# Optimization experiments

Hardware: AMD Instinct MI355X
Metric: run time of the kernel (lower is better)

The kernel has to match this reference:

```python
import jax, jax.numpy as jnp
import numpy as np

B, N, P, D = 32, 8, 6, 96
E, H, I, K, NL = 128, 8, 64, 32, 2
L = N * D  # transformer sequence length = 768
OUT = 128
EPS = 1e-5


def _layernorm(x, s, b):
    m = jnp.mean(x, axis=-1, keepdims=True)
    v = jnp.mean((x - m) ** 2, axis=-1, keepdims=True)
    return (x - m) / jnp.sqrt(v + EPS) * s + b


def _pos_encoding(length, d_model):
    pos = jnp.arange(length, dtype=jnp.float32)[:, None]
    div = jnp.exp(jnp.arange(0, d_model, 2, dtype=jnp.float32) * (-jnp.log(10000.0) / d_model))
    ang = pos * div  # [L, E/2]
    return jnp.stack([jnp.sin(ang), jnp.cos(ang)], axis=-1).reshape(length, d_model)


def setup_inputs() -> dict:
    key = jax.random.key(0)
    ks = jax.random.split(key, 20)
    s = 0.02
    return {
        "x": jax.random.normal(ks[0], (B, N, P, D), jnp.float32),
        "prototypes": jax.random.normal(ks[1], (D, K, P), jnp.float32),
        "emb_w": jax.random.normal(ks[2], (E, P), jnp.float32) * s,
        "emb_b": jnp.zeros((E,), jnp.float32),
        "proj_w": jax.random.normal(ks[3], (E, P), jnp.float32) * s,
        "proj_b": jnp.zeros((E,), jnp.float32),
        "in_proj_w": jax.random.normal(ks[4], (NL, 3 * E, E), jnp.float32) * s,
        "in_proj_b": jnp.zeros((NL, 3 * E), jnp.float32),
        "out_proj_w": jax.random.normal(ks[5], (NL, E, E), jnp.float32) * s,
        "out_proj_b": jnp.zeros((NL, E), jnp.float32),
        "ln1_s": jnp.ones((NL, E), jnp.float32),
        "ln1_b": jnp.zeros((NL, E), jnp.float32),
        "ffn_w1": jax.random.normal(ks[6], (NL, I, E), jnp.float32) * s,
        "ffn_b1": jnp.zeros((NL, I), jnp.float32),
        "ffn_w2": jax.random.normal(ks[7], (NL, E, I), jnp.float32) * s,
        "ffn_b2": jnp.zeros((NL, E), jnp.float32),
        "ln2_s": jnp.ones((NL, E), jnp.float32),
        "ln2_b": jnp.zeros((NL, E), jnp.float32),
        "out_w": jax.random.normal(ks[8], (OUT, L * E), jnp.float32) * s,
        "out_b": jnp.zeros((OUT,), jnp.float32),
    }


def reference(x, prototypes, emb_w, emb_b, proj_w, proj_b,
              in_proj_w, in_proj_b, out_proj_w, out_proj_b,
              ln1_s, ln1_b, ffn_w1, ffn_b1, ffn_w2, ffn_b2,
              ln2_s, ln2_b, out_w, out_b):
    # Faithful to torch .view: raw row-major reinterpretation [B,N,P,D] -> [B*N*D, P]
    x_flat = x.reshape(B * N * D, P)
    x_normed = x_flat / jnp.maximum(jnp.linalg.norm(x_flat, axis=1, keepdims=True), 1e-12)
    x_norm = x_normed.reshape(B, N, D, P)
    p_normed = prototypes / jnp.maximum(jnp.linalg.norm(prototypes, axis=2, keepdims=True), 1e-12)

    # Vectorized per-dim cosine-sim argmax + gather (replaces the Python loop over D)
    sim = jnp.einsum('bndp,dkp->bndk', x_norm, p_normed)  # [B,N,D,K]
    best_idx = jnp.argmax(sim, axis=3)                    # [B,N,D]
    d_idx = jnp.arange(D)[None, None, :]
    selected = p_normed[d_idx, best_idx]                  # [B,N,D,P]

    input_embed = (x_flat @ emb_w.T + emb_b).reshape(B, N, D, E)
    proto_embed = (selected.reshape(B * N * D, P) @ proj_w.T + proj_b).reshape(B, N, D, E)
    seq = (input_embed + proto_embed).reshape(B, L, E)
    seq = seq + _pos_encoding(L, E)[None]

    scale = 1.0 / jnp.sqrt(jnp.float32(E // H))
    for l in range(NL):
        qkv = seq @ in_proj_w[l].T + in_proj_b[l]          # [B,L,3E]
        q, k, v = jnp.split(qkv, 3, axis=-1)
        q = q.reshape(B, L, H, E // H)
        k = k.reshape(B, L, H, E // H)
        v = v.reshape(B, L, H, E // H)
        logits = jnp.einsum('blhd,bmhd->bhlm', q, k) * scale
        attn = jax.nn.softmax(logits, axis=-1)
        ctx = jnp.einsum('bhlm,bmhd->blhd', attn, v).reshape(B, L, E)
        attn_out = ctx @ out_proj_w[l].T + out_proj_b[l]
        seq = _layernorm(seq + attn_out, ln1_s[l], ln1_b[l])
        h = jax.nn.elu(seq @ ffn_w1[l].T + ffn_b1[l])
        ffn_out = h @ ffn_w2[l].T + ffn_b2[l]
        seq = _layernorm(seq + ffn_out, ln2_s[l], ln2_b[l])

    z = seq.reshape(B, L * E)
    return z @ out_w.T + out_b
```

## Files before the change

kernel.cpp:

```cpp
#include <hip/hip_runtime.h>
#include <hip/hip_bf16.h>
#include <math.h>

typedef unsigned short ushort_t;
typedef unsigned int uint_t;

#define BB 32
#define PP 6
#define DD 96
#define EE 128
#define HH 8
#define II 64
#define KK 32
#define LSEQ 768
#define ROWS (BB * LSEQ)
#define OUTN 128
#define KOUT (LSEQ * EE)

using bf16x8 = __attribute__((ext_vector_type(8))) short;
using bf16x4 = __attribute__((ext_vector_type(4))) short;
using f32x4  = __attribute__((ext_vector_type(4))) float;
using u32x4  = __attribute__((ext_vector_type(4))) uint_t;

__device__ __forceinline__ ushort_t f2b(float f) {
    __hip_bfloat16 h = __float2bfloat16(f);
    return *reinterpret_cast<ushort_t*>(&h);
}
__device__ __forceinline__ uint_t permpack(float hi, float lo) {
    return __builtin_amdgcn_perm(__builtin_bit_cast(uint_t, hi),
                                 __builtin_bit_cast(uint_t, lo), 0x07060302u);
}

#define NCAST 320
__global__ __launch_bounds__(512) void cast_embed_kernel(
    const float* __restrict__ s0, int n0, const float* __restrict__ s1, int n1,
    const float* __restrict__ s2, int n2, const float* __restrict__ s3, int n3,
    ushort_t* __restrict__ d0, ushort_t* __restrict__ d1,
    ushort_t* __restrict__ d2, ushort_t* __restrict__ d3,
    const float* __restrict__ x, const float* __restrict__ prot,
    const float* __restrict__ emb_w, const float* __restrict__ emb_b,
    const float* __restrict__ proj_w, const float* __restrict__ proj_b,
    float* __restrict__ seq, ushort_t* __restrict__ seq_bf)
{
    if (blockIdx.x < NCAST) {
        int i = blockIdx.x * 512 + threadIdx.x;
        if (i < n0) { d0[i] = f2b(s0[i]); return; }
        i -= n0;
        if (i < n1) { d1[i] = f2b(s1[i]); return; }
        i -= n1;
        if (i < n2) { d2[i] = f2b(s2[i]); return; }
        i -= n2;
        if (i < n3) { d3[i] = f2b(s3[i]); }
        return;
    }

    const int wave = threadIdx.x >> 6, lane = threadIdx.x & 63;
    const int r = (blockIdx.x - NCAST) * 8 + wave;
    const int d = r % DD;
    const int lpos = r % LSEQ;

    float xr[PP];
    float nx = 0.f;
    #pragma unroll
    for (int p = 0; p < PP; ++p) { xr[p] = x[r * PP + p]; nx += xr[p] * xr[p]; }
    const float xinv = 1.f / fmaxf(sqrtf(nx), 1e-12f);

    const int tk = lane & 31;
    const float* pr = prot + (d * KK + tk) * PP;
    float np2 = 0.f, dot = 0.f;
    #pragma unroll
    for (int p = 0; p < PP; ++p) {
        float pv = pr[p];
        np2 += pv * pv;
        dot += xr[p] * pv;
    }
    const float pinv = 1.f / fmaxf(sqrtf(np2), 1e-12f);
    float sim = dot * xinv * pinv;
    int k = tk;
    #pragma unroll
    for (int off = 16; off; off >>= 1) {
        float osim = __shfl_xor(sim, off);
        int   ok   = __shfl_xor(k, off);
        if (osim > sim || (osim == sim && ok < k)) { sim = osim; k = ok; }
    }
    const float* sr = prot + (d * KK + k) * PP;
    float sp[PP], sn2 = 0.f;
    #pragma unroll
    for (int p = 0; p < PP; ++p) { sp[p] = sr[p]; sn2 += sp[p] * sp[p]; }
    const float spinv = 1.f / fmaxf(sqrtf(sn2), 1e-12f);

    #pragma unroll
    for (int c = 0; c < 2; ++c) {
        const int t = lane + c * 64;
        float acc = emb_b[t] + proj_b[t];
        #pragma unroll
        for (int p = 0; p < PP; ++p) {
            acc = fmaf(xr[p], emb_w[t * PP + p], acc);
            acc = fmaf(sp[p] * spinv, proj_w[t * PP + p], acc);
        }
        const float twoj = (float)((t >> 1) * 2);
        const float div = __expf(twoj * (-9.210340371976184f / 128.0f));
        const float ang = (float)lpos * div;
        const float pe = (t & 1) ? __cosf(ang) : __sinf(ang);
        const float v = acc + pe;
        seq[(size_t)r * EE + t] = v;
        seq_bf[(size_t)r * EE + t] = f2b(v);
    }
}

__global__ __launch_bounds__(256) void gemm_qkv(
    const ushort_t* __restrict__ A, const ushort_t* __restrict__ W,
    const float* __restrict__ bias,
    ushort_t* __restrict__ q_bf, ushort_t* __restrict__ k2,
    ushort_t* __restrict__ v2)
{
    __shared__ ushort_t Ws[64 * 136];
    const int t = threadIdx.x;
    const int wave = t >> 6, lane = t & 63;
    const int quad = lane >> 4, l16 = lane & 15;
    const int m0 = blockIdx.y * 128, n0 = blockIdx.x * 64;

    for (int c = t; c < 64 * 16; c += 256) {
        int row = c >> 4, col = c & 15;
        *(bf16x8*)&Ws[row * 136 + col * 8] =
            *(const bf16x8*)&W[(size_t)(n0 + row) * 128 + col * 8];
    }
    __syncthreads();

    f32x4 acc[2][4];
    #pragma unroll
    for (int s = 0; s < 2; ++s)
        #pragma unroll
        for (int nt = 0; nt < 4; ++nt)
            acc[s][nt] = (f32x4){0.f, 0.f, 0.f, 0.f};

    const ushort_t* a0p = A + (size_t)(m0 + wave * 32 + l16) * 128 + quad * 8;
    const ushort_t* a1p = a0p + (size_t)16 * 128;
    const ushort_t* wp  = &Ws[l16 * 136 + quad * 8];

    #pragma unroll
    for (int k0 = 0; k0 < 128; k0 += 32) {
        bf16x8 a0 = *(const bf16x8*)(a0p + k0);
        bf16x8 a1 = *(const bf16x8*)(a1p + k0);
        #pragma unroll
        for (int nt = 0; nt < 4; ++nt) {
            bf16x8 wf = *(const bf16x8*)(wp + nt * 16 * 136 + k0);
            acc[0][nt] = __builtin_amdgcn_mfma_f32_16x16x32_bf16(wf, a0, acc[0][nt], 0, 0, 0);
            acc[1][nt] = __builtin_amdgcn_mfma_f32_16x16x32_bf16(wf, a1, acc[1][nt], 0, 0, 0);
        }
    }

    const int b = blockIdx.y / 6;
    #pragma unroll
    for (int s = 0; s < 2; ++s) {
        const int m = m0 + wave * 32 + s * 16 + l16;
        const int l = m - b * LSEQ;
        const int c32 = l >> 5, u = l & 31;
        #pragma unroll
        for (int nt = 0; nt < 4; ++nt) {
            const int nb = n0 + nt * 16 + quad * 4;
            float4 b4 = *(const float4*)&bias[nb];
            float v[4];
            #pragma unroll
            for (int r = 0; r < 4; ++r)
                v[r] = acc[s][nt][r] + ((const float*)&b4)[r];

            if (n0 < 128) {
                #pragma unroll
                for (int r = 0; r < 4; ++r) v[r] *= 0.36067376022224085f;
                uint2 w2;
                w2.x = permpack(v[1], v[0]);
                w2.y = permpack(v[3], v[2]);
                *(uint2*)&q_bf[(size_t)m * EE + nb] = w2;
            } else if (n0 < 256) {
                const int h = ((n0 - 128) >> 4) + nt;
                const int half = (u >> 2) & 1;
                const int mm = ((u >> 3) << 2) | (u & 3);
                uint2 w2;
                w2.x = permpack(v[1], v[0]);
                w2.y = permpack(v[3], v[2]);
                *(uint2*)&k2[((((((size_t)(b * HH + h)) * 24 + c32) * 2 + half) * 4 + quad) * 16 + mm) * 4] = w2;
            } else {
                const int h = ((n0 - 256) >> 4) + nt;
                const size_t vb = (((size_t)(b * HH + h)) * 24 + c32) * 512;
                #pragma unroll
                for (int r = 0; r < 4; ++r)
                    v2[vb + (quad * 4 + r) * 32 + u] = f2b(v[r]);
            }
        }
    }
}

__device__ __forceinline__ void attn_step32(
    bf16x4 kf0, bf16x4 kf1, bf16x8 vf, const bf16x4 (&qf)[2],
    f32x4 (&oacc)[2], f32x4 (&lacc)[2], bf16x8 ones8)
{
    const f32x4 zero4 = (f32x4){0.f, 0.f, 0.f, 0.f};
    #pragma unroll
    for (int s = 0; s < 2; ++s) {
        f32x4 sv0 = __builtin_amdgcn_mfma_f32_16x16x16bf16_1k(kf0, qf[s], zero4, 0, 0, 0);
        f32x4 sv1 = __builtin_amdgcn_mfma_f32_16x16x16bf16_1k(kf1, qf[s], zero4, 0, 0, 0);
        float e0 = __builtin_amdgcn_exp2f(sv0[0]);
        float e1 = __builtin_amdgcn_exp2f(sv0[1]);
        float e2 = __builtin_amdgcn_exp2f(sv0[2]);
        float e3 = __builtin_amdgcn_exp2f(sv0[3]);
        float e4 = __builtin_amdgcn_exp2f(sv1[0]);
        float e5 = __builtin_amdgcn_exp2f(sv1[1]);
        float e6 = __builtin_amdgcn_exp2f(sv1[2]);
        float e7 = __builtin_amdgcn_exp2f(sv1[3]);
        u32x4 pu;
        pu[0] = permpack(e1, e0);
        pu[1] = permpack(e3, e2);
        pu[2] = permpack(e5, e4);
        pu[3] = permpack(e7, e6);
        bf16x8 pf = __builtin_bit_cast(bf16x8, pu);
        oacc[s] = __builtin_amdgcn_mfma_f32_16x16x32_bf16(vf, pf, oacc[s], 0, 0, 0);
        lacc[s] = __builtin_amdgcn_mfma_f32_16x16x32_bf16(ones8, pf, lacc[s], 0, 0, 0);
    }
}

__global__ __launch_bounds__(256) void attention_mfma(
    const ushort_t* __restrict__ q_bf, const ushort_t* __restrict__ k2,
    const ushort_t* __restrict__ v2, ushort_t* __restrict__ ctx)
{
    const int bh = blockIdx.x;
    const int b = bh & 31, h = bh >> 5;
    const int qb = blockIdx.y;
    const int t = threadIdx.x;
    const int wave = t >> 6, lane = t & 63;
    const int quad = lane >> 4, l16 = lane & 15;
    const int hoff = h * 16;

    bf16x4 qf[2];
    #pragma unroll
    for (int s = 0; s < 2; ++s) {
        int row = b * LSEQ + qb * 128 + wave * 32 + s * 16 + l16;
        qf[s] = *(const bf16x4*)&q_bf[(size_t)row * EE + hoff + quad * 4];
    }

    const int bhn = b * HH + h;
    const ushort_t* kp = k2 + (size_t)bhn * 12288 + quad * 64 + l16 * 4;
    const ushort_t* vp = v2 + (size_t)bhn * 12288 + l16 * 32 + quad * 8;

    f32x4 oacc[2], lacc[2];
    oacc[0] = (f32x4){0.f, 0.f, 0.f, 0.f};
    oacc[1] = (f32x4){0.f, 0.f, 0.f, 0.f};
    lacc[0] = (f32x4){0.f, 0.f, 0.f, 0.f};
    lacc[1] = (f32x4){0.f, 0.f, 0.f, 0.f};
    bf16x8 ones8;
    #pragma unroll
    for (int j = 0; j < 8; ++j) ones8[j] = (short)0x3F80;

    bf16x4 k0a = *(const bf16x4*)(kp);
    bf16x4 k1a = *(const bf16x4*)(kp + 256);
    bf16x8 va  = *(const bf16x8*)(vp);
    bf16x4 k0b = *(const bf16x4*)(kp + 512);
    bf16x4 k1b = *(const bf16x4*)(kp + 768);
    bf16x8 vb  = *(const bf16x8*)(vp + 512);
    bf16x4 k0c = *(const bf16x4*)(kp + 1024);
    bf16x4 k1c = *(const bf16x4*)(kp + 1280);
    bf16x8 vc  = *(const bf16x8*)(vp + 1024);

    for (int c0 = 0; c0 < 24; c0 += 3) {
        attn_step32(k0a, k1a, va, qf, oacc, lacc, ones8);
        { int n = c0 + 3; if (n >= 24) n -= 24;
          k0a = *(const bf16x4*)(kp + n * 512);
          k1a = *(const bf16x4*)(kp + n * 512 + 256);
          va  = *(const bf16x8*)(vp + n * 512); }
        attn_step32(k0b, k1b, vb, qf, oacc, lacc, ones8);
        { int n = c0 + 4; if (n >= 24) n -= 24;
          k0b = *(const bf16x4*)(kp + n * 512);
          k1b = *(const bf16x4*)(kp + n * 512 + 256);
          vb  = *(const bf16x8*)(vp + n * 512); }
        attn_step32(k0c, k1c, vc, qf, oacc, lacc, ones8);
        { int n = c0 + 5; if (n >= 24) n -= 24;
          k0c = *(const bf16x4*)(kp + n * 512);
          k1c = *(const bf16x4*)(kp + n * 512 + 256);
          vc  = *(const bf16x8*)(vp + n * 512); }
    }

    #pragma unroll
    for (int s = 0; s < 2; ++s) {
        const float inv = 1.f / lacc[s][0];
        const int q = qb * 128 + wave * 32 + s * 16 + l16;
        uint2 w2;
        w2.x = permpack(oacc[s][1] * inv, oacc[s][0] * inv);
        w2.y = permpack(oacc[s][3] * inv, oacc[s][2] * inv);
        *(uint2*)&ctx[((size_t)(b * LSEQ + q)) * EE + hoff + quad * 4] = w2;
    }
}

#define W1OFF 0
#define W2OFF 8704
#define YOFF  17920
#define HOFF  26624
__global__ __launch_bounds__(256) void gemm_ln_ffn(
    const ushort_t* __restrict__ ctx_bf, const ushort_t* __restrict__ Wout,
    const float* __restrict__ bout,
    const float* __restrict__ g1, const float* __restrict__ be1,
    const ushort_t* __restrict__ W1, const float* __restrict__ b1,
    const ushort_t* __restrict__ W2, const float* __restrict__ b2,
    const float* __restrict__ g2, const float* __restrict__ be2,
    float* __restrict__ seq, ushort_t* __restrict__ seq_bf, int write_f32)
{
    __shared__ ushort_t S[31232];
    const int t = threadIdx.x;
    const int wave = t >> 6, lane = t & 63;
    const int quad = lane >> 4, l16 = lane & 15;
    const int m0 = blockIdx.x * 64;
    const int lrow = wave * 16 + l16;
    const int m = m0 + lrow;

    for (int c = t; c < 128 * 16; c += 256) {
        int row = c >> 4, col = c & 15;
        *(bf16x8*)&S[row * 136 + col * 8] =
            *(const bf16x8*)&Wout[(size_t)row * 128 + col * 8];
    }
    __syncthreads();

    f32x4 acc[8];
    #pragma unroll
    for (int nt = 0; nt < 8; ++nt) acc[nt] = (f32x4){0.f, 0.f, 0.f, 0.f};
    {
        const ushort_t* ap = ctx_bf + (size_t)m * EE + quad * 8;
        const ushort_t* wp = &S[l16 * 136 + quad * 8];
        #pragma unroll
        for (int k0 = 0; k0 < 128; k0 += 32) {
            bf16x8 a = *(const bf16x8*)(ap + k0);
            #pragma unroll
            for (int nt = 0; nt < 8; ++nt) {
                bf16x8 wf = *(const bf16x8*)(wp + nt * 16 * 136 + k0);
                acc[nt] = __builtin_amdgcn_mfma_f32_16x16x32_bf16(wf, a, acc[nt], 0, 0, 0);
            }
        }
    }
    __syncthreads();

    for (int c = t; c < 64 * 16; c += 256) {
        int row = c >> 4, col = c & 15;
        *(bf16x8*)&S[W1OFF + row * 136 + col * 8] =
            *(const bf16x8*)&W1[(size_t)row * 128 + col * 8];
    }
    for (int c = t; c < 128 * 8; c += 256) {
        int row = c >> 3, col = c & 7;
        *(bf16x8*)&S[W2OFF + row * 72 + col * 8] =
            *(const bf16x8*)&W2[(size_t)row * 64 + col * 8];
    }

    float y[8][4];
    float s = 0.f;
    #pragma unroll
    for (int nt = 0; nt < 8; ++nt) {
        const int nb = nt * 16 + quad * 4;
        float4 b4 = *(const float4*)&bout[nb];
        float4 r4 = *(const float4*)&seq[(size_t)m * EE + nb];
        #pragma unroll
        for (int r = 0; r < 4; ++r) {
            y[nt][r] = acc[nt][r] + ((const float*)&b4)[r] + ((const float*)&r4)[r];
            s += y[nt][r];
        }
    }
    s += __shfl_xor(s, 16);
    s += __shfl_xor(s, 32);
    float mean = s * (1.f / 128.f);
    float s2 = 0.f;
    #pragma unroll
    for (int nt = 0; nt < 8; ++nt)
        #pragma unroll
        for (int r = 0; r < 4; ++r) {
            float d = y[nt][r] - mean;
            s2 += d * d;
        }
    s2 += __shfl_xor(s2, 16);
    s2 += __shfl_xor(s2, 32);
    float rstd = 1.f / sqrtf(s2 * (1.f / 128.f) + 1e-5f);

    #pragma unroll
    for (int nt = 0; nt < 8; ++nt) {
        const int nb = nt * 16 + quad * 4;
        float4 g4 = *(const float4*)&g1[nb];
        float4 be4 = *(const float4*)&be1[nb];
        #pragma unroll
        for (int r = 0; r < 4; ++r)
            y[nt][r] = (y[nt][r] - mean) * rstd * ((const float*)&g4)[r] + ((const float*)&be4)[r];
        uint2 w2;
        w2.x = permpack(y[nt][1], y[nt][0]);
        w2.y = permpack(y[nt][3], y[nt][2]);
        *(uint2*)&S[YOFF + lrow * 136 + nb] = w2;
    }
    __syncthreads();

    f32x4 acc1[4];
    #pragma unroll
    for (int nt = 0; nt < 4; ++nt) acc1[nt] = (f32x4){0.f, 0.f, 0.f, 0.f};
    {
        const ushort_t* ap1 = &S[YOFF + lrow * 136 + quad * 8];
        const ushort_t* w1p = &S[W1OFF + l16 * 136 + quad * 8];
        #pragma unroll
        for (int k0 = 0; k0 < 128; k0 += 32) {
            bf16x8 a = *(const bf16x8*)(ap1 + k0);
            #pragma unroll
            for (int nt = 0; nt < 4; ++nt) {
                bf16x8 wf = *(const bf16x8*)(w1p + nt * 16 * 136 + k0);
                acc1[nt] = __builtin_amdgcn_mfma_f32_16x16x32_bf16(wf, a, acc1[nt], 0, 0, 0);
            }
        }
    }
    #pragma unroll
    for (int nt = 0; nt < 4; ++nt) {
        const int ib = nt * 16 + quad * 4;
        float4 b4 = *(const float4*)&b1[ib];
        float hv[4];
        #pragma unroll
        for (int r = 0; r < 4; ++r) {
            float u = acc1[nt][r] + ((const float*)&b4)[r];
            hv[r] = u > 0.f ? u : expm1f(u);
        }
        uint2 w2;
        w2.x = permpack(hv[1], hv[0]);
        w2.y = permpack(hv[3], hv[2]);
        *(uint2*)&S[HOFF + lrow * 72 + ib] = w2;
    }

    f32x4 acc2[8];
    #pragma unroll
    for (int nt = 0; nt < 8; ++nt) acc2[nt] = (f32x4){0.f, 0.f, 0.f, 0.f};
    {
        const ushort_t* hp  = &S[HOFF + lrow * 72 + quad * 8];
        const ushort_t* w2p = &S[W2OFF + l16 * 72 + quad * 8];
        #pragma unroll
        for (int k0 = 0; k0 < 64; k0 += 32) {
            bf16x8 hf = *(const bf16x8*)(hp + k0);
            #pragma unroll
            for (int nt = 0; nt < 8; ++nt) {
                bf16x8 wf = *(const bf16x8*)(w2p + nt * 16 * 72 + k0);
                acc2[nt] = __builtin_amdgcn_mfma_f32_16x16x32_bf16(wf, hf, acc2[nt], 0, 0, 0);
            }
        }
    }

    float v[8][4];
    s = 0.f;
    #pragma unroll
    for (int nt = 0; nt < 8; ++nt) {
        const int nb = nt * 16 + quad * 4;
        float4 b4 = *(const float4*)&b2[nb];
        #pragma unroll
        for (int r = 0; r < 4; ++r) {
            v[nt][r] = acc2[nt][r] + ((const float*)&b4)[r] + y[nt][r];
            s += v[nt][r];
        }
    }
    s += __shfl_xor(s, 16);
    s += __shfl_xor(s, 32);
    mean = s * (1.f / 128.f);
    s2 = 0.f;
    #pragma unroll
    for (int nt = 0; nt < 8; ++nt)
        #pragma unroll
        for (int r = 0; r < 4; ++r) {
            float d = v[nt][r] - mean;
            s2 += d * d;
        }
    s2 += __shfl_xor(s2, 16);
    s2 += __shfl_xor(s2, 32);
    rstd = 1.f / sqrtf(s2 * (1.f / 128.f) + 1e-5f);

    #pragma unroll
    for (int nt = 0; nt < 8; ++nt) {
        const int nb = nt * 16 + quad * 4;
        float4 g4 = *(const float4*)&g2[nb];
        float4 be4 = *(const float4*)&be2[nb];
        float o[4];
        #pragma unroll
        for (int r = 0; r < 4; ++r)
            o[r] = (v[nt][r] - mean) * rstd * ((const float*)&g4)[r] + ((const float*)&be4)[r];
        if (write_f32) {
            float4 f4 = {o[0], o[1], o[2], o[3]};
            *(float4*)&seq[(size_t)m * EE + nb] = f4;
        }
        uint2 w2;
        w2.x = permpack(o[1], o[0]);
        w2.y = permpack(o[3], o[2]);
        *(uint2*)&seq_bf[(size_t)m * EE + nb] = w2;
    }
}

#define PKC 384
#define PNBLK (KOUT / PKC)
__global__ __launch_bounds__(256) void out_gemm3(
    const ushort_t* __restrict__ seqbf, const float* __restrict__ out_w,
    float* __restrict__ part)
{
    const int t = threadIdx.x;
    const int wave = t >> 6, lane = t & 63;
    const int quad = lane >> 4, l16 = lane & 15;
    const size_t k0 = (size_t)blockIdx.x * PKC;
    const int n0 = wave * 32;

    f32x4 acc[2][2];
    #pragma unroll
    for (int mt = 0; mt < 2; ++mt)
        #pragma unroll
        for (int nt = 0; nt < 2; ++nt)
            acc[mt][nt] = (f32x4){0.f, 0.f, 0.f, 0.f};

    const ushort_t* a0p = seqbf + (size_t)l16 * KOUT + k0 + quad * 8;
    const ushort_t* a1p = a0p + (size_t)16 * KOUT;
    const float* w0p = out_w + (size_t)(n0 + l16) * KOUT + k0 + quad * 8;
    const float* w1p = w0p + (size_t)16 * KOUT;

    for (int ks = 0; ks < PKC; ks += 32) {
        bf16x8 a0 = *(const bf16x8*)(a0p + ks);
        bf16x8 a1 = *(const bf16x8*)(a1p + ks);
        float4 wa0 = *(const float4*)(w0p + ks);
        float4 wa1 = *(const float4*)(w0p + ks + 4);
        float4 wb0 = *(const float4*)(w1p + ks);
        float4 wb1 = *(const float4*)(w1p + ks + 4);
        u32x4 b0, b1;
        b0[0] = permpack(wa0.y, wa0.x); b0[1] = permpack(wa0.w, wa0.z);
        b0[2] = permpack(wa1.y, wa1.x); b0[3] = permpack(wa1.w, wa1.z);
        b1[0] = permpack(wb0.y, wb0.x); b1[1] = permpack(wb0.w, wb0.z);
        b1[2] = permpack(wb1.y, wb1.x); b1[3] = permpack(wb1.w, wb1.z);
        bf16x8 bf0 = __builtin_bit_cast(bf16x8, b0);
        bf16x8 bf1 = __builtin_bit_cast(bf16x8, b1);
        acc[0][0] = __builtin_amdgcn_mfma_f32_16x16x32_bf16(a0, bf0, acc[0][0], 0, 0, 0);
        acc[1][0] = __builtin_amdgcn_mfma_f32_16x16x32_bf16(a1, bf0, acc[1][0], 0, 0, 0);
        acc[0][1] = __builtin_amdgcn_mfma_f32_16x16x32_bf16(a0, bf1, acc[0][1], 0, 0, 0);
        acc[1][1] = __builtin_amdgcn_mfma_f32_16x16x32_bf16(a1, bf1, acc[1][1], 0, 0, 0);
    }

    float* pb = part + (size_t)blockIdx.x * (32 * 128);
    #pragma unroll
    for (int mt = 0; mt < 2; ++mt)
        #pragma unroll
        for (int nt = 0; nt < 2; ++nt)
            #pragma unroll
            for (int r = 0; r < 4; ++r)
                pb[(mt * 16 + quad * 4 + r) * 128 + n0 + nt * 16 + l16] = acc[mt][nt][r];
}

__global__ __launch_bounds__(256) void out_reduce1(
    const float* __restrict__ part, float* __restrict__ part2)
{
    const int g = blockIdx.x & 15, sp = blockIdx.x >> 4;
    const int i = g * 256 + threadIdx.x;
    const float* p = part + (size_t)sp * 32 * 4096 + i;
    float s0 = 0.f, s1 = 0.f, s2 = 0.f, s3 = 0.f;
    for (int blk = 0; blk < 32; blk += 4) {
        s0 += p[(size_t)blk * 4096];
        s1 += p[(size_t)(blk + 1) * 4096];
        s2 += p[(size_t)(blk + 2) * 4096];
        s3 += p[(size_t)(blk + 3) * 4096];
    }
    part2[sp * 4096 + i] = (s0 + s1) + (s2 + s3);
}

__global__ __launch_bounds__(256) void out_reduce2(
    const float* __restrict__ part2, const float* __restrict__ out_b,
    float* __restrict__ out)
{
    const int i = blockIdx.x * 256 + threadIdx.x;
    float s = 0.f;
    #pragma unroll
    for (int sp = 0; sp < 8; ++sp) s += part2[sp * 4096 + i];
    out[i] = out_b[i & (OUTN - 1)] + s;
}

extern "C" void kernel_launch(void* const* d_in, const int* in_sizes, int n_in,
                              void* d_out, int out_size, void* d_ws, size_t ws_size,
                              hipStream_t stream)
{
    const float* x          = (const float*)d_in[0];
    const float* prototypes = (const float*)d_in[1];
    const float* emb_w      = (const float*)d_in[2];
    const float* emb_b      = (const float*)d_in[3];
    const float* proj_w     = (const float*)d_in[4];
    const float* proj_b     = (const float*)d_in[5];
    const float* in_proj_w  = (const float*)d_in[6];
    const float* in_proj_b  = (const float*)d_in[7];
    const float* out_proj_w = (const float*)d_in[8];
    const float* out_proj_b = (const float*)d_in[9];
    const float* ln1_s      = (const float*)d_in[10];
    const float* ln1_b      = (const float*)d_in[11];
    const float* ffn_w1     = (const float*)d_in[12];
    const float* ffn_b1     = (const float*)d_in[13];
    const float* ffn_w2     = (const float*)d_in[14];
    const float* ffn_b2     = (const float*)d_in[15];
    const float* ln2_s      = (const float*)d_in[16];
    const float* ln2_b      = (const float*)d_in[17];
    const float* out_w      = (const float*)d_in[18];
    const float* out_b      = (const float*)d_in[19];
    float* out = (float*)d_out;
    char* base = (char*)d_ws;

    float*    seq    = (float*)base;
    float*    tmp    = (float*)(base + 12582912);
    ushort_t* seq_bf = (ushort_t*)(base + 25165824);
    ushort_t* q_bf   = (ushort_t*)(base + 31457280);
    ushort_t* k2     = (ushort_t*)(base + 37748736);
    ushort_t* v2     = (ushort_t*)(base + 44040192);
    ushort_t* ctx_bf = (ushort_t*)(base + 50331648);
    ushort_t* w_bf   = (ushort_t*)(base + 56623104);
    float*    part   = tmp;
    float*    part2  = (float*)(base + 12582912 + 8388608);
    (void)ws_size;

    ushort_t* w_in  = w_bf;
    ushort_t* w_out = w_bf + 98304;
    ushort_t* w_f1  = w_bf + 131072;
    ushort_t* w_f2  = w_bf + 147456;

    cast_embed_kernel<<<NCAST + ROWS / 8, 512, 0, stream>>>(
        in_proj_w, 98304, out_proj_w, 32768, ffn_w1, 16384, ffn_w2, 16384,
        w_in, w_out, w_f1, w_f2,
        x, prototypes, emb_w, emb_b, proj_w, proj_b, seq, seq_bf);

    for (int l = 0; l < 2; ++l) {
        gemm_qkv<<<dim3(6, 192), 256, 0, stream>>>(
            seq_bf, w_in + (size_t)l * 49152, in_proj_b + l * 384,
            q_bf, k2, v2);
        attention_mfma<<<dim3(BB * HH, 6), 256, 0, stream>>>(q_bf, k2, v2, ctx_bf);
        gemm_ln_ffn<<<ROWS / 64, 256, 0, stream>>>(
            ctx_bf, w_out + (size_t)l * 16384, out_proj_b + l * 128,
            ln1_s + l * EE, ln1_b + l * EE,
            w_f1 + (size_t)l * 8192, ffn_b1 + l * II,
            w_f2 + (size_t)l * 8192, ffn_b2 + l * EE,
            ln2_s + l * EE, ln2_b + l * EE,
            seq, seq_bf, l == 0 ? 1 : 0);
    }

    out_gemm3<<<PNBLK, 256, 0, stream>>>(seq_bf, out_w, part);
    out_reduce1<<<128, 256, 0, stream>>>(part, part2);
    out_reduce2<<<BB * OUTN / 256, 256, 0, stream>>>(part2, out_b, out);
}
```

Measured before the change: 260.9 us.

## Drop fp32 residual stream, read weights from global, merge output reductions

The fp32 copy of the sequence is removed, so the residual is read back from the bf16 buffer and the extra fp32 writes and reads go away. The QKV and FFN GEMMs now load weight fragments straight from global memory (L1/L2 cached) instead of staging them in LDS. This removes barriers and shrinks shared memory, which may raise occupancy. The two output reduction kernels are merged into one that reduces through shared memory, saving a launch and a round trip. The residual now carries bf16 rounding, which slightly reduces accuracy.

Result: slower. 291.1 us (+11.5%).

```diff
diff --git a/kernel.cpp b/kernel.cpp
--- a/kernel.cpp
+++ b/kernel.cpp
@@ -30,6 +30,12 @@
     return __builtin_amdgcn_perm(__builtin_bit_cast(uint_t, hi),
                                  __builtin_bit_cast(uint_t, lo), 0x07060302u);
 }
+__device__ __forceinline__ float blo(uint_t u) {
+    return __builtin_bit_cast(float, u << 16);
+}
+__device__ __forceinline__ float bhi(uint_t u) {
+    return __builtin_bit_cast(float, u & 0xffff0000u);
+}
 
 #define NCAST 320
 __global__ __launch_bounds__(512) void cast_embed_kernel(
@@ -40,7 +46,7 @@
     const float* __restrict__ x, const float* __restrict__ prot,
     const float* __restrict__ emb_w, const float* __restrict__ emb_b,
     const float* __restrict__ proj_w, const float* __restrict__ proj_b,
-    float* __restrict__ seq, ushort_t* __restrict__ seq_bf)
+    ushort_t* __restrict__ seq_bf)
 {
     if (blockIdx.x < NCAST) {
         int i = blockIdx.x * 512 + threadIdx.x;
@@ -102,9 +108,7 @@
         const float div = __expf(twoj * (-9.210340371976184f / 128.0f));
         const float ang = (float)lpos * div;
         const float pe = (t & 1) ? __cosf(ang) : __sinf(ang);
-        const float v = acc + pe;
-        seq[(size_t)r * EE + t] = v;
-        seq_bf[(size_t)r * EE + t] = f2b(v);
+        seq_bf[(size_t)r * EE + t] = f2b(acc + pe);
     }
 }
 
@@ -114,19 +118,11 @@
     ushort_t* __restrict__ q_bf, ushort_t* __restrict__ k2,
     ushort_t* __restrict__ v2)
 {
-    __shared__ ushort_t Ws[64 * 136];
     const int t = threadIdx.x;
     const int wave = t >> 6, lane = t & 63;
     const int quad = lane >> 4, l16 = lane & 15;
     const int m0 = blockIdx.y * 128, n0 = blockIdx.x * 64;
 
-    for (int c = t; c < 64 * 16; c += 256) {
-        int row = c >> 4, col = c & 15;
-        *(bf16x8*)&Ws[row * 136 + col * 8] =
-            *(const bf16x8*)&W[(size_t)(n0 + row) * 128 + col * 8];
-    }
-    __syncthreads();
-
     f32x4 acc[2][4];
     #pragma unroll
     for (int s = 0; s < 2; ++s)
@@ -136,7 +132,7 @@
 
     const ushort_t* a0p = A + (size_t)(m0 + wave * 32 + l16) * 128 + quad * 8;
     const ushort_t* a1p = a0p + (size_t)16 * 128;
-    const ushort_t* wp  = &Ws[l16 * 136 + quad * 8];
+    const ushort_t* wp  = W + (size_t)(n0 + l16) * 128 + quad * 8;
 
     #pragma unroll
     for (int k0 = 0; k0 < 128; k0 += 32) {
@@ -144,7 +140,7 @@
         bf16x8 a1 = *(const bf16x8*)(a1p + k0);
         #pragma unroll
         for (int nt = 0; nt < 4; ++nt) {
-            bf16x8 wf = *(const bf16x8*)(wp + nt * 16 * 136 + k0);
+            bf16x8 wf = *(const bf16x8*)(wp + nt * 16 * 128 + k0);
             acc[0][nt] = __builtin_amdgcn_mfma_f32_16x16x32_bf16(wf, a0, acc[0][nt], 0, 0, 0);
             acc[1][nt] = __builtin_amdgcn_mfma_f32_16x16x32_bf16(wf, a1, acc[1][nt], 0, 0, 0);
         }
@@ -290,10 +286,7 @@
     }
 }
 
-#define W1OFF 0
-#define W2OFF 8704
-#define YOFF  17920
-#define HOFF  26624
+#define YHOFF 8704
 __global__ __launch_bounds__(256) void gemm_ln_ffn(
     const ushort_t* __restrict__ ctx_bf, const ushort_t* __restrict__ Wout,
     const float* __restrict__ bout,
@@ -301,9 +294,9 @@
     const ushort_t* __restrict__ W1, const float* __restrict__ b1,
     const ushort_t* __restrict__ W2, const float* __restrict__ b2,
     const float* __restrict__ g2, const float* __restrict__ be2,
-    float* __restrict__ seq, ushort_t* __restrict__ seq_bf, int write_f32)
-{
-    __shared__ ushort_t S[31232];
+    ushort_t* __restrict__ seq_bf)
+{
+    __shared__ ushort_t S[13312];
     const int t = threadIdx.x;
     const int wave = t >> 6, lane = t & 63;
     const int quad = lane >> 4, l16 = lane & 15;
@@ -311,40 +304,21 @@
     const int lrow = wave * 16 + l16;
     const int m = m0 + lrow;
 
-    for (int c = t; c < 128 * 16; c += 256) {
-        int row = c >> 4, col = c & 15;
-        *(bf16x8*)&S[row * 136 + col * 8] =
-            *(const bf16x8*)&Wout[(size_t)row * 128 + col * 8];
-    }
-    __syncthreads();
-
     f32x4 acc[8];
     #pragma unroll
     for (int nt = 0; nt < 8; ++nt) acc[nt] = (f32x4){0.f, 0.f, 0.f, 0.f};
     {
         const ushort_t* ap = ctx_bf + (size_t)m * EE + quad * 8;
-        const ushort_t* wp = &S[l16 * 136 + quad * 8];
+        const ushort_t* wp = Wout + (size_t)l16 * 128 + quad * 8;
         #pragma unroll
         for (int k0 = 0; k0 < 128; k0 += 32) {
             bf16x8 a = *(const bf16x8*)(ap + k0);
             #pragma unroll
             for (int nt = 0; nt < 8; ++nt) {
-                bf16x8 wf = *(const bf16x8*)(wp + nt * 16 * 136 + k0);
+                bf16x8 wf = *(const bf16x8*)(wp + nt * 16 * 128 + k0);
                 acc[nt] = __builtin_amdgcn_mfma_f32_16x16x32_bf16(wf, a, acc[nt], 0, 0, 0);
             }
         }
-    }
-    __syncthreads();
-
-    for (int c = t; c < 64 * 16; c += 256) {
-        int row = c >> 4, col = c & 15;
-        *(bf16x8*)&S[W1OFF + row * 136 + col * 8] =
-            *(const bf16x8*)&W1[(size_t)row * 128 + col * 8];
-    }
-    for (int c = t; c < 128 * 8; c += 256) {
-        int row = c >> 3, col = c & 7;
-        *(bf16x8*)&S[W2OFF + row * 72 + col * 8] =
-            *(const bf16x8*)&W2[(size_t)row * 64 + col * 8];
     }
 
     float y[8][4];
@@ -353,10 +327,11 @@
     for (int nt = 0; nt < 8; ++nt) {
         const int nb = nt * 16 + quad * 4;
         float4 b4 = *(const float4*)&bout[nb];
-        float4 r4 = *(const float4*)&seq[(size_t)m * EE + nb];
+        uint2 rr = *(const uint2*)&seq_bf[(size_t)m * EE + nb];
+        float rv[4] = {blo(rr.x), bhi(rr.x), blo(rr.y), bhi(rr.y)};
         #pragma unroll
         for (int r = 0; r < 4; ++r) {
-            y[nt][r] = acc[nt][r] + ((const float*)&b4)[r] + ((const float*)&r4)[r];
+            y[nt][r] = acc[nt][r] + ((const float*)&b4)[r] + rv[r];
             s += y[nt][r];
         }
     }
@@ -386,22 +361,21 @@
         uint2 w2;
         w2.x = permpack(y[nt][1], y[nt][0]);
         w2.y = permpack(y[nt][3], y[nt][2]);
-        *(uint2*)&S[YOFF + lrow * 136 + nb] = w2;
-    }
-    __syncthreads();
+        *(uint2*)&S[lrow * 136 + nb] = w2;
+    }
 
     f32x4 acc1[4];
     #pragma unroll
     for (int nt = 0; nt < 4; ++nt) acc1[nt] = (f32x4){0.f, 0.f, 0.f, 0.f};
     {
-        const ushort_t* ap1 = &S[YOFF + lrow * 136 + quad * 8];
-        const ushort_t* w1p = &S[W1OFF + l16 * 136 + quad * 8];
+        const ushort_t* ap1 = &S[lrow * 136 + quad * 8];
+        const ushort_t* w1p = W1 + (size_t)l16 * 128 + quad * 8;
         #pragma unroll
         for (int k0 = 0; k0 < 128; k0 += 32) {
             bf16x8 a = *(const bf16x8*)(ap1 + k0);
             #pragma unroll
             for (int nt = 0; nt < 4; ++nt) {
-                bf16x8 wf = *(const bf16x8*)(w1p + nt * 16 * 136 + k0);
+                bf16x8 wf = *(const bf16x8*)(w1p + nt * 16 * 128 + k0);
                 acc1[nt] = __builtin_amdgcn_mfma_f32_16x16x32_bf16(wf, a, acc1[nt], 0, 0, 0);
             }
         }
@@ -419,21 +393,21 @@
         uint2 w2;
         w2.x = permpack(hv[1], hv[0]);
         w2.y = permpack(hv[3], hv[2]);
-        *(uint2*)&S[HOFF + lrow * 72 + ib] = w2;
+        *(uint2*)&S[YHOFF + lrow * 72 + ib] = w2;
     }
 
     f32x4 acc2[8];
     #pragma unroll
     for (int nt = 0; nt < 8; ++nt) acc2[nt] = (f32x4){0.f, 0.f, 0.f, 0.f};
     {
-        const ushort_t* hp  = &S[HOFF + lrow * 72 + quad * 8];
-        const ushort_t* w2p = &S[W2OFF + l16 * 72 + quad * 8];
+        const ushort_t* hp  = &S[YHOFF + lrow * 72 + quad * 8];
+        const ushort_t* w2p = W2 + (size_t)l16 * 64 + quad * 8;
         #pragma unroll
         for (int k0 = 0; k0 < 64; k0 += 32) {
             bf16x8 hf = *(const bf16x8*)(hp + k0);
             #pragma unroll
             for (int nt = 0; nt < 8; ++nt) {
-                bf16x8 wf = *(const bf16x8*)(w2p + nt * 16 * 72 + k0);
+                bf16x8 wf = *(const bf16x8*)(w2p + nt * 16 * 64 + k0);
                 acc2[nt] = __builtin_amdgcn_mfma_f32_16x16x32_bf16(wf, hf, acc2[nt], 0, 0, 0);
             }
         }
@@ -475,10 +449,6 @@
         #pragma unroll
         for (int r = 0; r < 4; ++r)
             o[r] = (v[nt][r] - mean) * rstd * ((const float*)&g4)[r] + ((const float*)&be4)[r];
-        if (write_f32) {
-            float4 f4 = {o[0], o[1], o[2], o[3]};
-            *(float4*)&seq[(size_t)m * EE + nb] = f4;
-        }
         uint2 w2;
         w2.x = permpack(o[1], o[0]);
         w2.y = permpack(o[3], o[2]);
@@ -540,12 +510,14 @@
                 pb[(mt * 16 + quad * 4 + r) * 128 + n0 + nt * 16 + l16] = acc[mt][nt][r];
 }
 
-__global__ __launch_bounds__(256) void out_reduce1(
-    const float* __restrict__ part, float* __restrict__ part2)
-{
-    const int g = blockIdx.x & 15, sp = blockIdx.x >> 4;
-    const int i = g * 256 + threadIdx.x;
-    const float* p = part + (size_t)sp * 32 * 4096 + i;
+__global__ __launch_bounds__(256) void out_reduce(
+    const float* __restrict__ part, const float* __restrict__ out_b,
+    float* __restrict__ out)
+{
+    __shared__ float red[8][32];
+    const int g = threadIdx.x & 31, sub = threadIdx.x >> 5;
+    const int i = blockIdx.x * 32 + g;
+    const float* p = part + (size_t)sub * 32 * 4096 + i;
     float s0 = 0.f, s1 = 0.f, s2 = 0.f, s3 = 0.f;
     for (int blk = 0; blk < 32; blk += 4) {
         s0 += p[(size_t)blk * 4096];
@@ -553,18 +525,14 @@
         s2 += p[(size_t)(blk + 2) * 4096];
         s3 += p[(size_t)(blk + 3) * 4096];
     }
-    part2[sp * 4096 + i] = (s0 + s1) + (s2 + s3);
-}
-
-__global__ __launch_bounds__(256) void out_reduce2(
-    const float* __restrict__ part2, const float* __restrict__ out_b,
-    float* __restrict__ out)
-{
-    const int i = blockIdx.x * 256 + threadIdx.x;
-    float s = 0.f;
-    #pragma unroll
-    for (int sp = 0; sp < 8; ++sp) s += part2[sp * 4096 + i];
-    out[i] = out_b[i & (OUTN - 1)] + s;
+    red[sub][g] = (s0 + s1) + (s2 + s3);
+    __syncthreads();
+    if (sub == 0) {
+        float s = 0.f;
+        #pragma unroll
+        for (int j = 0; j < 8; ++j) s += red[j][g];
+        out[i] = out_b[i & (OUTN - 1)] + s;
+    }
 }
 
 extern "C" void kernel_launch(void* const* d_in, const int* in_sizes, int n_in,
@@ -594,16 +562,13 @@
     float* out = (float*)d_out;
     char* base = (char*)d_ws;
 
-    float*    seq    = (float*)base;
-    float*    tmp    = (float*)(base + 12582912);
+    float*    part   = (float*)base;
     ushort_t* seq_bf = (ushort_t*)(base + 25165824);
     ushort_t* q_bf   = (ushort_t*)(base + 31457280);
     ushort_t* k2     = (ushort_t*)(base + 37748736);
     ushort_t* v2     = (ushort_t*)(base + 44040192);
     ushort_t* ctx_bf = (ushort_t*)(base + 50331648);
     ushort_t* w_bf   = (ushort_t*)(base + 56623104);
-    float*    part   = tmp;
-    float*    part2  = (float*)(base + 12582912 + 8388608);
     (void)ws_size;
 
     ushort_t* w_in  = w_bf;
@@ -614,7 +579,7 @@
     cast_embed_kernel<<<NCAST + ROWS / 8, 512, 0, stream>>>(
         in_proj_w, 98304, out_proj_w, 32768, ffn_w1, 16384, ffn_w2, 16384,
         w_in, w_out, w_f1, w_f2,
-        x, prototypes, emb_w, emb_b, proj_w, proj_b, seq, seq_bf);
+        x, prototypes, emb_w, emb_b, proj_w, proj_b, seq_bf);
 
     for (int l = 0; l < 2; ++l) {
         gemm_qkv<<<dim3(6, 192), 256, 0, stream>>>(
@@ -627,10 +592,9 @@
             w_f1 + (size_t)l * 8192, ffn_b1 + l * II,
             w_f2 + (size_t)l * 8192, ffn_b2 + l * EE,
             ln2_s + l * EE, ln2_b + l * EE,
-            seq, seq_bf, l == 0 ? 1 : 0);
+            seq_bf);
     }
 
     out_gemm3<<<PNBLK, 256, 0, stream>>>(seq_bf, out_w, part);
-    out_reduce1<<<128, 256, 0, stream>>>(part, part2);
-    out_reduce2<<<BB * OUTN / 256, 256, 0, stream>>>(part2, out_b, out);
-}
+    out_reduce<<<OUTN * BB / 32, 256, 0, stream>>>(part, out_b, out);
+}
```
